# Kernel optimization log

Hardware: AMD Instinct MI355X
Metric: run time of the kernel (lower is better)

The kernel has to match this reference:

```python
import jax, jax.numpy as jnp
import numpy as np

N_NODES = 100000


def _gcn_conv(x, W, b, row, col, norm, n_nodes):
    # PyG GCNConv: h = x @ W; out[i] = sum_{(j->i)} norm_e * h[j] + b
    h = x @ W
    msg = h[row] * norm[:, None]              # [E_tot, out_dim] gather
    out = jax.ops.segment_sum(msg, col, num_segments=n_nodes)  # scatter-add
    return out + b


def _norm_and_loops(edge_index, n_nodes):
    # add self loops, compute symmetric normalization deg^-1/2 * deg^-1/2
    loop = jnp.arange(n_nodes, dtype=edge_index.dtype)
    row = jnp.concatenate([edge_index[0], loop])
    col = jnp.concatenate([edge_index[1], loop])
    deg = jax.ops.segment_sum(jnp.ones_like(col, dtype=jnp.float32), col,
                              num_segments=n_nodes)
    dis = jnp.where(deg > 0, jax.lax.rsqrt(jnp.maximum(deg, 1.0)), 0.0)
    norm = dis[row] * dis[col]
    return row, col, norm


def setup_inputs() -> dict:
    key = jax.random.key(0)
    ks = jax.random.split(key, 9)
    in_c, hid, lat = 128, 128, 64
    n_edges = 1600000
    x = jax.random.normal(ks[0], (N_NODES, in_c), dtype=jnp.float32)
    edge_index = jax.random.randint(ks[1], (2, n_edges), 0, N_NODES, dtype=jnp.int64)
    s1 = 1.0 / np.sqrt(in_c)
    s2 = 1.0 / np.sqrt(hid)
    W1 = jax.random.uniform(ks[2], (in_c, hid), jnp.float32, -s1, s1)
    b1 = jnp.zeros((hid,), jnp.float32)
    W_mu = jax.random.uniform(ks[3], (hid, lat), jnp.float32, -s2, s2)
    b_mu = jnp.zeros((lat,), jnp.float32)
    W_lv = jax.random.uniform(ks[4], (hid, lat), jnp.float32, -s2, s2)
    b_lv = jnp.zeros((lat,), jnp.float32)
    eps = jax.random.normal(ks[5], (N_NODES, lat), dtype=jnp.float32)
    return {"x": x, "edge_index": edge_index, "W1": W1, "b1": b1,
            "W_mu": W_mu, "b_mu": b_mu, "W_lv": W_lv, "b_lv": b_lv,
            "eps": eps}


def reference(x, edge_index, W1, b1, W_mu, b_mu, W_lv, b_lv, eps):
    row, col, norm = _norm_and_loops(edge_index, N_NODES)
    h = jax.nn.relu(_gcn_conv(x, W1, b1, row, col, norm, N_NODES))
    mu = _gcn_conv(h, W_mu, b_mu, row, col, norm, N_NODES)
    logvar = _gcn_conv(h, W_lv, b_lv, row, col, norm, N_NODES)
    # reparameterize (training mode): z = mu + eps * exp(0.5*logvar)
    z = mu + eps * jnp.exp(0.5 * logvar)
    return (z, mu, logvar)
```

## Files before the change

### kernel.cpp

```cpp
#include <hip/hip_runtime.h>
#include <math.h>


#define SHIFT 9
#define EPB 4096
#define HEPB 8192
#define CAP 15104

using f32x4 = __attribute__((ext_vector_type(4))) float;
using f16x8 = __attribute__((ext_vector_type(8))) _Float16;
using f16x2 = __attribute__((ext_vector_type(2))) _Float16;

__device__ inline int scan256(int v, int* wsum) {
    __syncthreads();
    int lane = threadIdx.x & 63, wid = threadIdx.x >> 6;
    int s = v;
#pragma unroll
    for (int d = 1; d < 64; d <<= 1) {
        int u = __shfl_up(s, d, 64);
        if (lane >= d) s += u;
    }
    if (lane == 63) wsum[wid] = s;
    __syncthreads();
    int off = 0;
    for (int w = 0; w < wid; w++) off += wsum[w];
    return off + s - v;
}

__global__ __launch_bounds__(256) void k_bhist(const int* __restrict__ coli,
                                               int* __restrict__ gbh,
                                               int E, int NB) {
    __shared__ int lh[256];
    int t = threadIdx.x;
    lh[t] = 0;
    __syncthreads();
    int base = blockIdx.x * HEPB;
    for (int i = t; i < HEPB; i += 256) {
        int e = base + i;
        if (e < E) atomicAdd(&lh[coli[e] >> SHIFT], 1);
    }
    __syncthreads();
    if (t < NB && lh[t]) atomicAdd(&gbh[t], lh[t]);
}

__global__ __launch_bounds__(256) void k_bscan(const int* __restrict__ gbh,
                                               int* __restrict__ bptr,
                                               int* __restrict__ bcur,
                                               int NB, int E,
                                               int* __restrict__ rowptr, int N) {
    __shared__ int wsum[4];
    int t = threadIdx.x;
    int v = (t < NB) ? gbh[t] : 0;
    int e = scan256(v, wsum);
    if (t < NB) { bptr[t] = e; bcur[t] = e; }
    if (t == 0) { bptr[NB] = E; rowptr[N] = E; }
}

__global__ __launch_bounds__(256) void k_bucket(const int* __restrict__ rowi,
                                                const int* __restrict__ coli,
                                                int* __restrict__ bcur,
                                                int2* __restrict__ recs,
                                                int E, int NB) {
    __shared__ int lh[256], excl[256], lcur[256], gbase[256], wsum[4];
    __shared__ int2 stage[EPB];
    int t = threadIdx.x;
    lh[t] = 0;
    __syncthreads();
    int base = blockIdx.x * EPB;
    int nE = min(EPB, E - base);
    int2 my[16];
    int cnt = 0;
#pragma unroll
    for (int i = 0; i < 16; i++) {
        int idx = t + i * 256;
        if (idx < nE) {
            my[cnt].x = rowi[base + idx];
            my[cnt].y = coli[base + idx];
            atomicAdd(&lh[my[cnt].y >> SHIFT], 1);
            cnt++;
        }
    }
    __syncthreads();
    int myh = lh[t];
    int ex = scan256(myh, wsum);
    excl[t] = ex;
    lcur[t] = ex;
    if (t < NB && myh) gbase[t] = atomicAdd(&bcur[t], myh);
    __syncthreads();
    for (int i = 0; i < cnt; i++) {
        int p = atomicAdd(&lcur[my[i].y >> SHIFT], 1);
        stage[p] = my[i];
    }
    __syncthreads();
    for (int i = t; i < nE; i += 256) {
        int2 r = stage[i];
        int bb = r.y >> SHIFT;
        recs[gbase[bb] + (i - excl[bb])] = r;
    }
}

__global__ __launch_bounds__(256) void k_fill2(const int2* __restrict__ recs,
                                               const int* __restrict__ bptr,
                                               int* __restrict__ rowptr,
                                               float* __restrict__ dis,
                                               int* __restrict__ srcs, int N) {
    __shared__ int hist[512], excl[512], wsum[4];
    __shared__ int srcsL[CAP];
    int t = threadIdx.x;
    int b = blockIdx.x;
    int nbase = b << SHIFT;
    int start = bptr[b], end = bptr[b + 1];
    int cnt = end - start;
    hist[t] = 0;
    hist[t + 256] = 0;
    __syncthreads();
    for (int i = start + t; i < end; i += 256)
        atomicAdd(&hist[recs[i].y - nbase], 1);
    __syncthreads();
    int h0 = hist[2 * t], h1 = hist[2 * t + 1];
    int e0 = scan256(h0 + h1, wsum);
    excl[2 * t] = e0;
    excl[2 * t + 1] = e0 + h0;
    int n0 = nbase + 2 * t, n1 = nbase + 2 * t + 1;
    if (n0 < N) { rowptr[n0] = start + e0;      dis[n0] = rsqrtf((float)(h0 + 1)); }
    if (n1 < N) { rowptr[n1] = start + e0 + h0; dis[n1] = rsqrtf((float)(h1 + 1)); }
    __syncthreads();
    if (cnt <= CAP) {
        for (int i = start + t; i < end; i += 256) {
            int2 r = recs[i];
            int p = atomicAdd(&excl[r.y - nbase], 1);
            srcsL[p] = r.x;
        }
        __syncthreads();
        for (int i = t; i < cnt; i += 256) srcs[start + i] = srcsL[i];
    } else {
        for (int i = start + t; i < end; i += 256) {
            int2 r = recs[i];
            int p = atomicAdd(&excl[r.y - nbase], 1);
            srcs[start + p] = r.x;
        }
    }
}

template <bool XF16>
__global__ __launch_bounds__(256) void k_gemm(const void* __restrict__ Xv,
                                              const float* __restrict__ Wa,
                                              const float* __restrict__ Wb,
                                              int split,
                                              const float* __restrict__ dis,
                                              _Float16* __restrict__ Y,
                                              int M, int ngroups) {
    __shared__ _Float16 Wl[16384];
    int tid = threadIdx.x;
    int wbs = 128 - split;
    for (int i = tid; i < 16384; i += 256) {
        int k = i >> 7, n = i & 127;
        float v = (n < split) ? Wa[k * split + n] : Wb[k * wbs + (n - split)];
        int tt = n >> 4, c = (k >> 5), q = (k >> 3) & 3, ln = q * 16 + (n & 15);
        Wl[(((tt * 4 + c) * 64) + ln) * 8 + (k & 7)] = (_Float16)v;
    }
    __syncthreads();

    int lane = tid & 63, w = tid >> 6;
    f16x8 B[32];
#pragma unroll
    for (int i = 0; i < 32; i++)
        B[i] = *(const f16x8*)&Wl[(i * 64 + lane) * 8];

    int m16 = lane & 15, quad = lane >> 4;
    for (int g = blockIdx.x; g < ngroups; g += gridDim.x) {
        int rowbase = g * 64 + w * 16;
        if (rowbase >= M) continue;
        int arow = min(rowbase + m16, M - 1);
        f16x8 A[4];
        if (XF16) {
            const _Float16* X = (const _Float16*)Xv;
#pragma unroll
            for (int c = 0; c < 4; c++)
                A[c] = *(const f16x8*)&X[arow * 128 + c * 32 + quad * 8];
        } else {
            const float* X = (const float*)Xv;
#pragma unroll
            for (int c = 0; c < 4; c++) {
                float4 u0 = *(const float4*)&X[arow * 128 + c * 32 + quad * 8];
                float4 u1 = *(const float4*)&X[arow * 128 + c * 32 + quad * 8 + 4];
                f16x8 a;
                a[0] = (_Float16)u0.x; a[1] = (_Float16)u0.y;
                a[2] = (_Float16)u0.z; a[3] = (_Float16)u0.w;
                a[4] = (_Float16)u1.x; a[5] = (_Float16)u1.y;
                a[6] = (_Float16)u1.z; a[7] = (_Float16)u1.w;
                A[c] = a;
            }
        }

        f32x4 acc[8];
#pragma unroll
        for (int t = 0; t < 8; t++) acc[t] = (f32x4)(0.f);
#pragma unroll
        for (int t = 0; t < 8; t++)
#pragma unroll
            for (int c = 0; c < 4; c++)
                acc[t] = __builtin_amdgcn_mfma_f32_16x16x32_f16(
                    A[c], B[t * 4 + c], acc[t], 0, 0, 0);

#pragma unroll
        for (int r = 0; r < 4; r++) {
            int row = rowbase + quad * 4 + r;
            if (row < M) {
                float d = dis[row];
#pragma unroll
                for (int t = 0; t < 8; t++)
                    Y[row * 128 + t * 16 + m16] = (_Float16)(d * acc[t][r]);
            }
        }
    }
}

template <bool OF16>
__global__ __launch_bounds__(256) void k_agg(const f16x2* __restrict__ F,
                                             const float* __restrict__ dis,
                                             const int* __restrict__ rowptr,
                                             const int* __restrict__ srcs,
                                             const float* __restrict__ ba,
                                             const float* __restrict__ bb,
                                             void* __restrict__ outA,
                                             void* __restrict__ outB,
                                             int N) {
    int node = blockIdx.x * 4 + (threadIdx.x >> 6);
    if (node >= N) return;
    int lane = threadIdx.x & 63;
    f16x2 sv = F[node * 64 + lane];
    float ax = (float)sv[0];
    float ay = (float)sv[1];
    int s = rowptr[node], e = rowptr[node + 1];
    int t = s;
    for (; t + 4 <= e; t += 4) {
        int i0 = srcs[t + 0], i1 = srcs[t + 1];
        int i2 = srcs[t + 2], i3 = srcs[t + 3];
        f16x2 f0 = F[i0 * 64 + lane];
        f16x2 f1 = F[i1 * 64 + lane];
        f16x2 f2 = F[i2 * 64 + lane];
        f16x2 f3 = F[i3 * 64 + lane];
        ax += (float)f0[0] + (float)f1[0] + (float)f2[0] + (float)f3[0];
        ay += (float)f0[1] + (float)f1[1] + (float)f2[1] + (float)f3[1];
    }
    for (; t < e; t++) {
        int sr = srcs[t];
        f16x2 f = F[sr * 64 + lane];
        ax += (float)f[0];
        ay += (float)f[1];
    }
    float di = dis[node];
    int j = lane << 1;
    if (OF16) {
        float o0 = fmaxf(fmaf(di, ax, ba[j]), 0.f);
        float o1 = fmaxf(fmaf(di, ay, ba[j + 1]), 0.f);
        f16x2 o;
        o[0] = (_Float16)o0;
        o[1] = (_Float16)o1;
        ((f16x2*)outA)[node * 64 + lane] = o;
    } else {
        float* op;
        int jj;
        const float* bp;
        if (j < 64) { op = (float*)outA; jj = j; bp = ba; }
        else        { op = (float*)outB; jj = j - 64; bp = bb; }
        float o0 = fmaf(di, ax, bp[jj]);
        float o1 = fmaf(di, ay, bp[jj + 1]);
        *(float2*)&op[node * 64 + jj] = make_float2(o0, o1);
    }
}

__global__ __launch_bounds__(256) void k_final(const float* __restrict__ mu,
                                               const float* __restrict__ lv,
                                               const float* __restrict__ eps,
                                               float* __restrict__ z, int n) {
    int i = blockIdx.x * 256 + threadIdx.x;
    if (i < n) z[i] = fmaf(eps[i], expf(0.5f * lv[i]), mu[i]);
}

extern "C" void kernel_launch(void* const* d_in, const int* in_sizes, int n_in,
                              void* d_out, int out_size, void* d_ws, size_t ws_size,
                              hipStream_t stream) {
    const float* x   = (const float*)d_in[0];
    const int*   ei  = (const int*)d_in[1];
    const float* W1  = (const float*)d_in[2];
    const float* b1  = (const float*)d_in[3];
    const float* Wmu = (const float*)d_in[4];
    const float* bmu = (const float*)d_in[5];
    const float* Wlv = (const float*)d_in[6];
    const float* blv = (const float*)d_in[7];
    const float* eps = (const float*)d_in[8];

    int N = in_sizes[0] / 128;
    int E = in_sizes[1] / 2;
    const int* rowi = ei;
    const int* coli = ei + E;
    int NB = (N + (1 << SHIFT) - 1) >> SHIFT;

    char* ws = (char*)d_ws;
    size_t off = 0;
    auto alloc = [&](size_t bytes) -> void* {
        void* p = ws + off;
        off += (bytes + 255) & ~(size_t)255;
        return p;
    };
    _Float16* bufA = (_Float16*)alloc((size_t)N * 128 * 2);
    _Float16* bufB = (_Float16*)alloc((size_t)N * 128 * 2);
    float* dis    = (float*)alloc((size_t)N * 4);
    int*   rowptr = (int*)alloc((size_t)(N + 1) * 4);
    int*   srcs   = (int*)alloc((size_t)E * 4);
    int2*  recs   = (int2*)alloc((size_t)E * 8);
    int*   bhist  = (int*)alloc((size_t)NB * 4);
    int*   bptr   = (int*)alloc((size_t)(NB + 1) * 4);
    int*   bcur   = (int*)alloc((size_t)NB * 4);

    float* zo  = (float*)d_out;
    float* muo = zo + (size_t)N * 64;
    float* lvo = zo + (size_t)N * 128;

    hipMemsetAsync(bhist, 0, (size_t)NB * 4, stream);
    k_bhist<<<(E + HEPB - 1) / HEPB, 256, 0, stream>>>(coli, bhist, E, NB);
    k_bscan<<<1, 256, 0, stream>>>(bhist, bptr, bcur, NB, E, rowptr, N);
    k_bucket<<<(E + EPB - 1) / EPB, 256, 0, stream>>>(rowi, coli, bcur, recs, E, NB);
    k_fill2<<<NB, 256, 0, stream>>>(recs, bptr, rowptr, dis, srcs, N);

    int ngroups = (N + 63) / 64;
    int gblk = ngroups < 640 ? ngroups : 640;
    k_gemm<false><<<gblk, 256, 0, stream>>>(x, W1, W1, 128, dis, bufA, N, ngroups);
    k_agg<true><<<(N + 3) / 4, 256, 0, stream>>>((const f16x2*)bufA, dis, rowptr,
                                                 srcs, b1, b1, bufB, bufB, N);
    k_gemm<true><<<gblk, 256, 0, stream>>>(bufB, Wmu, Wlv, 64, dis, bufA, N, ngroups);
    k_agg<false><<<(N + 3) / 4, 256, 0, stream>>>((const f16x2*)bufA, dis, rowptr,
                                                  srcs, bmu, blv, muo, lvo, N);
    k_final<<<((N * 64) + 255) / 256, 256, 0, stream>>>(muo, lvo, eps, zo, N * 64);
}
```

Measured before the change: 434.9 us.

## Widen aggregation gathers, fuse reparameterization, and privatize bucket histograms per wave

The aggregation kernel now has each wavefront split into four 16-lane groups, each gathering a full 128-wide f16 neighbor row with 16-byte loads. The per-group partial sums are combined with cross-lane shuffles, which lets the loop handle four or eight edges per step with fewer, wider memory transactions. The z = mu + eps*exp(0.5*logvar) step moves into the second aggregation kernel, removing the separate final kernel and its re-read of mu/logvar. The histogram and bucketing kernels use per-wave shared histograms to cut LDS atomic contention, and bucketing uses half the block size and reloads inputs instead of holding them in registers, which costs a second global read of the edge arrays.

```diff
diff --git a/kernel.cpp b/kernel.cpp
--- a/kernel.cpp
+++ b/kernel.cpp
@@ -3,7 +3,7 @@
 
 
 #define SHIFT 9
-#define EPB 4096
+#define EPB 2048
 #define HEPB 8192
 #define CAP 15104
 
@@ -30,17 +30,20 @@
 __global__ __launch_bounds__(256) void k_bhist(const int* __restrict__ coli,
                                                int* __restrict__ gbh,
                                                int E, int NB) {
-    __shared__ int lh[256];
-    int t = threadIdx.x;
-    lh[t] = 0;
+    __shared__ int lh[4][256];
+    int t = threadIdx.x, w = t >> 6;
+    lh[0][t] = 0; lh[1][t] = 0; lh[2][t] = 0; lh[3][t] = 0;
     __syncthreads();
     int base = blockIdx.x * HEPB;
     for (int i = t; i < HEPB; i += 256) {
         int e = base + i;
-        if (e < E) atomicAdd(&lh[coli[e] >> SHIFT], 1);
-    }
-    __syncthreads();
-    if (t < NB && lh[t]) atomicAdd(&gbh[t], lh[t]);
+        if (e < E) atomicAdd(&lh[w][coli[e] >> SHIFT], 1);
+    }
+    __syncthreads();
+    if (t < NB) {
+        int v = lh[0][t] + lh[1][t] + lh[2][t] + lh[3][t];
+        if (v) atomicAdd(&gbh[t], v);
+    }
 }
 
 __global__ __launch_bounds__(256) void k_bscan(const int* __restrict__ gbh,
@@ -61,35 +64,30 @@
                                                 int* __restrict__ bcur,
                                                 int2* __restrict__ recs,
                                                 int E, int NB) {
-    __shared__ int lh[256], excl[256], lcur[256], gbase[256], wsum[4];
+    __shared__ int lh[4][256], lcur[4][256], excl[256], gbase[256], wsum[4];
     __shared__ int2 stage[EPB];
-    int t = threadIdx.x;
-    lh[t] = 0;
+    int t = threadIdx.x, w = t >> 6;
+    lh[0][t] = 0; lh[1][t] = 0; lh[2][t] = 0; lh[3][t] = 0;
     __syncthreads();
     int base = blockIdx.x * EPB;
     int nE = min(EPB, E - base);
-    int2 my[16];
-    int cnt = 0;
-#pragma unroll
-    for (int i = 0; i < 16; i++) {
-        int idx = t + i * 256;
-        if (idx < nE) {
-            my[cnt].x = rowi[base + idx];
-            my[cnt].y = coli[base + idx];
-            atomicAdd(&lh[my[cnt].y >> SHIFT], 1);
-            cnt++;
-        }
-    }
-    __syncthreads();
-    int myh = lh[t];
-    int ex = scan256(myh, wsum);
+    for (int i = t; i < nE; i += 256)
+        atomicAdd(&lh[w][coli[base + i] >> SHIFT], 1);
+    __syncthreads();
+    int h0 = lh[0][t], h1 = lh[1][t], h2 = lh[2][t], h3 = lh[3][t];
+    int tot = h0 + h1 + h2 + h3;
+    int ex = scan256(tot, wsum);
     excl[t] = ex;
-    lcur[t] = ex;
-    if (t < NB && myh) gbase[t] = atomicAdd(&bcur[t], myh);
-    __syncthreads();
-    for (int i = 0; i < cnt; i++) {
-        int p = atomicAdd(&lcur[my[i].y >> SHIFT], 1);
-        stage[p] = my[i];
+    lcur[0][t] = ex;
+    lcur[1][t] = ex + h0;
+    lcur[2][t] = ex + h0 + h1;
+    lcur[3][t] = ex + h0 + h1 + h2;
+    if (t < NB && tot) gbase[t] = atomicAdd(&bcur[t], tot);
+    __syncthreads();
+    for (int i = t; i < nE; i += 256) {
+        int r = rowi[base + i], c = coli[base + i];
+        int p = atomicAdd(&lcur[w][c >> SHIFT], 1);
+        stage[p] = make_int2(r, c);
     }
     __syncthreads();
     for (int i = t; i < nE; i += 256) {
@@ -217,7 +215,7 @@
 }
 
 template <bool OF16>
-__global__ __launch_bounds__(256) void k_agg(const f16x2* __restrict__ F,
+__global__ __launch_bounds__(256) void k_agg(const _Float16* __restrict__ F,
                                              const float* __restrict__ dis,
                                              const int* __restrict__ rowptr,
                                              const int* __restrict__ srcs,
@@ -225,58 +223,116 @@
                                              const float* __restrict__ bb,
                                              void* __restrict__ outA,
                                              void* __restrict__ outB,
-                                             int N) {
+                                             const float* __restrict__ eps,
+                                             float* __restrict__ z, int N) {
     int node = blockIdx.x * 4 + (threadIdx.x >> 6);
     if (node >= N) return;
     int lane = threadIdx.x & 63;
-    f16x2 sv = F[node * 64 + lane];
-    float ax = (float)sv[0];
-    float ay = (float)sv[1];
+    int g = lane >> 4, sl = lane & 15;
+    const f16x8* Fr = (const f16x8*)F;
+
+    float acc[8];
+#pragma unroll
+    for (int j = 0; j < 8; j++) acc[j] = 0.f;
+    if (g == 0) {
+        f16x8 v = Fr[node * 16 + sl];
+#pragma unroll
+        for (int j = 0; j < 8; j++) acc[j] = (float)v[j];
+    }
+
     int s = rowptr[node], e = rowptr[node + 1];
     int t = s;
-    for (; t + 4 <= e; t += 4) {
-        int i0 = srcs[t + 0], i1 = srcs[t + 1];
-        int i2 = srcs[t + 2], i3 = srcs[t + 3];
-        f16x2 f0 = F[i0 * 64 + lane];
-        f16x2 f1 = F[i1 * 64 + lane];
-        f16x2 f2 = F[i2 * 64 + lane];
-        f16x2 f3 = F[i3 * 64 + lane];
-        ax += (float)f0[0] + (float)f1[0] + (float)f2[0] + (float)f3[0];
-        ay += (float)f0[1] + (float)f1[1] + (float)f2[1] + (float)f3[1];
-    }
-    for (; t < e; t++) {
-        int sr = srcs[t];
-        f16x2 f = F[sr * 64 + lane];
-        ax += (float)f[0];
-        ay += (float)f[1];
-    }
+    for (; t + 8 <= e; t += 8) {
+        int i0 = srcs[t + g];
+        int i1 = srcs[t + 4 + g];
+        f16x8 v0 = Fr[i0 * 16 + sl];
+        f16x8 v1 = Fr[i1 * 16 + sl];
+#pragma unroll
+        for (int j = 0; j < 8; j++)
+            acc[j] += (float)v0[j] + (float)v1[j];
+    }
+    if (t + 4 <= e) {
+        int i0 = srcs[t + g];
+        f16x8 v0 = Fr[i0 * 16 + sl];
+#pragma unroll
+        for (int j = 0; j < 8; j++) acc[j] += (float)v0[j];
+        t += 4;
+    }
+    if (t < e) {
+        int idx = t + g;
+        bool ok = idx < e;
+        int i0 = ok ? srcs[idx] : 0;
+        f16x8 v0 = Fr[i0 * 16 + sl];
+        if (ok) {
+#pragma unroll
+            for (int j = 0; j < 8; j++) acc[j] += (float)v0[j];
+        }
+    }
+
+#pragma unroll
+    for (int j = 0; j < 8; j++) {
+        acc[j] += __shfl_xor(acc[j], 16);
+        acc[j] += __shfl_xor(acc[j], 32);
+    }
+
     float di = dis[node];
-    int j = lane << 1;
-    if (OF16) {
-        float o0 = fmaxf(fmaf(di, ax, ba[j]), 0.f);
-        float o1 = fmaxf(fmaf(di, ay, ba[j + 1]), 0.f);
-        f16x2 o;
-        o[0] = (_Float16)o0;
-        o[1] = (_Float16)o1;
-        ((f16x2*)outA)[node * 64 + lane] = o;
+    if constexpr (OF16) {
+        float4 b0 = *(const float4*)&ba[sl * 8];
+        float4 b1 = *(const float4*)&ba[sl * 8 + 4];
+        if (lane < 16) {
+            f16x8 o;
+            o[0] = (_Float16)fmaxf(fmaf(di, acc[0], b0.x), 0.f);
+            o[1] = (_Float16)fmaxf(fmaf(di, acc[1], b0.y), 0.f);
+            o[2] = (_Float16)fmaxf(fmaf(di, acc[2], b0.z), 0.f);
+            o[3] = (_Float16)fmaxf(fmaf(di, acc[3], b0.w), 0.f);
+            o[4] = (_Float16)fmaxf(fmaf(di, acc[4], b1.x), 0.f);
+            o[5] = (_Float16)fmaxf(fmaf(di, acc[5], b1.y), 0.f);
+            o[6] = (_Float16)fmaxf(fmaf(di, acc[6], b1.z), 0.f);
+            o[7] = (_Float16)fmaxf(fmaf(di, acc[7], b1.w), 0.f);
+            ((f16x8*)outA)[node * 16 + sl] = o;
+        }
     } else {
-        float* op;
-        int jj;
-        const float* bp;
-        if (j < 64) { op = (float*)outA; jj = j; bp = ba; }
-        else        { op = (float*)outB; jj = j - 64; bp = bb; }
-        float o0 = fmaf(di, ax, bp[jj]);
-        float o1 = fmaf(di, ay, bp[jj + 1]);
-        *(float2*)&op[node * 64 + jj] = make_float2(o0, o1);
-    }
-}
-
-__global__ __launch_bounds__(256) void k_final(const float* __restrict__ mu,
-                                               const float* __restrict__ lv,
-                                               const float* __restrict__ eps,
-                                               float* __restrict__ z, int n) {
-    int i = blockIdx.x * 256 + threadIdx.x;
-    if (i < n) z[i] = fmaf(eps[i], expf(0.5f * lv[i]), mu[i]);
+        const float* bp = (sl < 8) ? ba : bb;
+        int cb = (sl & 7) * 8;
+        float4 b0 = *(const float4*)&bp[cb];
+        float4 b1 = *(const float4*)&bp[cb + 4];
+        float o[8];
+        o[0] = fmaf(di, acc[0], b0.x);
+        o[1] = fmaf(di, acc[1], b0.y);
+        o[2] = fmaf(di, acc[2], b0.z);
+        o[3] = fmaf(di, acc[3], b0.w);
+        o[4] = fmaf(di, acc[4], b1.x);
+        o[5] = fmaf(di, acc[5], b1.y);
+        o[6] = fmaf(di, acc[6], b1.z);
+        o[7] = fmaf(di, acc[7], b1.w);
+        if (lane < 16) {
+            float* op = (sl < 8) ? (float*)outA : (float*)outB;
+            f32x4 s0, s1;
+            s0[0] = o[0]; s0[1] = o[1]; s0[2] = o[2]; s0[3] = o[3];
+            s1[0] = o[4]; s1[1] = o[5]; s1[2] = o[6]; s1[3] = o[7];
+            __builtin_nontemporal_store(s0, (f32x4*)&op[node * 64 + cb]);
+            __builtin_nontemporal_store(s1, (f32x4*)&op[node * 64 + cb + 4]);
+        }
+        float lvv[8];
+#pragma unroll
+        for (int j = 0; j < 8; j++) lvv[j] = __shfl_xor(o[j], 8);
+        if (lane < 8) {
+            int zb = node * 64 + sl * 8;
+            float4 e0 = *(const float4*)&eps[zb];
+            float4 e1 = *(const float4*)&eps[zb + 4];
+            f32x4 z0, z1;
+            z0[0] = fmaf(e0.x, expf(0.5f * lvv[0]), o[0]);
+            z0[1] = fmaf(e0.y, expf(0.5f * lvv[1]), o[1]);
+            z0[2] = fmaf(e0.z, expf(0.5f * lvv[2]), o[2]);
+            z0[3] = fmaf(e0.w, expf(0.5f * lvv[3]), o[3]);
+            z1[0] = fmaf(e1.x, expf(0.5f * lvv[4]), o[4]);
+            z1[1] = fmaf(e1.y, expf(0.5f * lvv[5]), o[5]);
+            z1[2] = fmaf(e1.z, expf(0.5f * lvv[6]), o[6]);
+            z1[3] = fmaf(e1.w, expf(0.5f * lvv[7]), o[7]);
+            __builtin_nontemporal_store(z0, (f32x4*)&z[zb]);
+            __builtin_nontemporal_store(z1, (f32x4*)&z[zb + 4]);
+        }
+    }
 }
 
 extern "C" void kernel_launch(void* const* d_in, const int* in_sizes, int n_in,
@@ -328,10 +384,11 @@
     int ngroups = (N + 63) / 64;
     int gblk = ngroups < 640 ? ngroups : 640;
     k_gemm<false><<<gblk, 256, 0, stream>>>(x, W1, W1, 128, dis, bufA, N, ngroups);
-    k_agg<true><<<(N + 3) / 4, 256, 0, stream>>>((const f16x2*)bufA, dis, rowptr,
-                                                 srcs, b1, b1, bufB, bufB, N);
+    k_agg<true><<<(N + 3) / 4, 256, 0, stream>>>(bufA, dis, rowptr, srcs,
+                                                 b1, b1, bufB, bufB,
+                                                 nullptr, nullptr, N);
     k_gemm<true><<<gblk, 256, 0, stream>>>(bufB, Wmu, Wlv, 64, dis, bufA, N, ngroups);
-    k_agg<false><<<(N + 3) / 4, 256, 0, stream>>>((const f16x2*)bufA, dis, rowptr,
-                                                  srcs, bmu, blv, muo, lvo, N);
-    k_final<<<((N * 64) + 255) / 256, 256, 0, stream>>>(muo, lvo, eps, zo, N * 64);
-}
+    k_agg<false><<<(N + 3) / 4, 256, 0, stream>>>(bufA, dis, rowptr, srcs,
+                                                  bmu, blv, muo, lvo,
+                                                  eps, zo, N);
+}
```

New measurement: 409.9 us. 1.06x faster.
